# Performance work log

Measured on AMD Instinct MI355X. Metric: run time of the kernel, lower is better.

The kernel has to match this reference:

```python
import jax, jax.numpy as jnp
import numpy as np

N_EMB = 1024
N_HEAD = 16
HEAD_SIZE = N_EMB // N_HEAD  # 64
B, T = 4, 4096


def setup_inputs() -> dict:
    key = jax.random.key(0)
    kx, kq, kk, kv = jax.random.split(key, 4)
    x = jax.random.normal(kx, (B, T, N_EMB), dtype=jnp.float32)
    # torch nn.Linear(in=N_EMB, out=HEAD_SIZE, bias=False) weight: [out, in]
    s = 1.0 / np.sqrt(N_EMB)
    Wq = jax.random.uniform(kq, (HEAD_SIZE, N_EMB), jnp.float32, -s, s)
    Wk = jax.random.uniform(kk, (HEAD_SIZE, N_EMB), jnp.float32, -s, s)
    Wv = jax.random.uniform(kv, (HEAD_SIZE, N_EMB), jnp.float32, -s, s)
    return {"x": x, "Wq": Wq, "Wk": Wk, "Wv": Wv}


def reference(x, Wq, Wk, Wv):
    # q,k,v: [B,T,H]
    q = jnp.einsum('btc,hc->bth', x, Wq)
    k = jnp.einsum('btc,hc->bth', x, Wk)
    v = jnp.einsum('btc,hc->bth', x, Wv)
    scale = HEAD_SIZE ** (-0.5)
    att = jnp.einsum('bth,bsh->bts', q, k) * scale  # [B,T,T]
    Tn = x.shape[1]
    causal = jnp.tril(jnp.ones((Tn, Tn), dtype=bool))
    att = jnp.where(causal, att, -jnp.inf)
    att = jax.nn.softmax(att, axis=-1)
    # dropout p=0.0 -> identity
    out = jnp.einsum('bts,bsh->bth', att, v)  # [B,T,H]
    return out
```

## Files before the change

### kernel.cpp

```cpp
#include <hip/hip_runtime.h>


typedef __attribute__((ext_vector_type(8))) short v8s;
typedef __attribute__((ext_vector_type(4))) float v4f;

static __device__ __forceinline__ unsigned short f2bf(float x) {
  unsigned int u = __builtin_bit_cast(unsigned int, x);
  u += 0x7fffu + ((u >> 16) & 1u);
  return (unsigned short)(u >> 16);
}

static __device__ __forceinline__ void dma16(const void* src, void* dst) {
  __builtin_amdgcn_global_load_lds(
      (const __attribute__((address_space(1))) void*)src,
      (__attribute__((address_space(3))) void*)dst, 16, 0, 0);
}

__global__ __launch_bounds__(256) void pack_w(const float* __restrict__ Wq,
                                              const float* __restrict__ Wk,
                                              const float* __restrict__ Wv,
                                              unsigned short* __restrict__ WF) {
  int idx = (blockIdx.x * 256 + threadIdx.x) * 4;
  int row = idx >> 10;
  int k   = idx & 1023;
  const float* src;
  float scale;
  if (row < 64)       { src = Wq + row * 1024 + k;         scale = 0.125f; }
  else if (row < 128) { src = Wk + (row - 64) * 1024 + k;  scale = 1.0f;   }
  else                { src = Wv + (row - 128) * 1024 + k; scale = 1.0f;   }
  float4 f = *(const float4*)src;
  ushort4 o;
  o.x = f2bf(f.x * scale); o.y = f2bf(f.y * scale);
  o.z = f2bf(f.z * scale); o.w = f2bf(f.w * scale);
  size_t off = ((size_t)(k >> 5) * 12 + (row >> 4)) * 512 +
               (((k >> 3) & 3) * 16 + (row & 15)) * 8 + (k & 7);
  *(ushort4*)(WF + off) = o;
}

__global__ __launch_bounds__(256) void qkv(const float* __restrict__ x,
                                           const unsigned short* __restrict__ WF,
                                           unsigned short* __restrict__ Qg,
                                           unsigned short* __restrict__ KF,
                                           unsigned short* __restrict__ VF) {
  __shared__ alignas(16) char xs[2][32768];
  const int tid   = threadIdx.x;
  const int lane  = tid & 63;
  const int wv    = tid >> 6;
  const int quad  = lane >> 4;
  const int colid = lane & 15;
  const int row0  = blockIdx.x * 64;

  const char* xB = (const char*)x;
  const unsigned short* wf = WF + lane * 8;

  v4f acc[12];
#pragma unroll
  for (int i = 0; i < 12; i++) acc[i] = (v4f){0.f, 0.f, 0.f, 0.f};

  auto stage = [&](int kt, int slot) {
#pragma unroll
    for (int i = 0; i < 8; i++) {
      int id = wv * 8 + i;
      int s = (id >> 1) & 3, h = id & 1;
      const char* src = xB + (size_t)(row0 + wv * 16 + colid) * 4096 +
                        kt * 512 + s * 128 + quad * 32 + h * 16;
      dma16(src, &xs[slot][id * 1024]);
    }
  };

  stage(0, 0);

  for (int kt = 0; kt < 8; kt++) {
    const int slot = kt & 1;
    __syncthreads();
    if (kt < 7) stage(kt + 1, slot ^ 1);
#pragma unroll
    for (int s = 0; s < 4; s++) {
      const int g = kt * 4 + s;
      v8s bw[3];
#pragma unroll
      for (int ntl = 0; ntl < 3; ntl++)
        bw[ntl] = *(const v8s*)(wf + ((size_t)g * 12 + wv * 3 + ntl) * 512);
#pragma unroll
      for (int mg = 0; mg < 4; mg++) {
        float4 f0 = *(const float4*)(&xs[slot][(mg * 8 + s * 2 + 0) * 1024 + lane * 16]);
        float4 f1 = *(const float4*)(&xs[slot][(mg * 8 + s * 2 + 1) * 1024 + lane * 16]);
        v8s a;
        a[0] = (short)f2bf(f0.x); a[1] = (short)f2bf(f0.y);
        a[2] = (short)f2bf(f0.z); a[3] = (short)f2bf(f0.w);
        a[4] = (short)f2bf(f1.x); a[5] = (short)f2bf(f1.y);
        a[6] = (short)f2bf(f1.z); a[7] = (short)f2bf(f1.w);
#pragma unroll
        for (int ntl = 0; ntl < 3; ntl++)
          acc[mg * 3 + ntl] =
              __builtin_amdgcn_mfma_f32_16x16x32_bf16(a, bw[ntl], acc[mg * 3 + ntl], 0, 0, 0);
      }
    }
  }

#pragma unroll
  for (int ntl = 0; ntl < 3; ntl++) {
    const int nt = wv * 3 + ntl;
#pragma unroll
    for (int mg = 0; mg < 4; mg++) {
      const int trow_base = row0 + mg * 16 + quad * 4;
      if (nt < 4) {
#pragma unroll
        for (int r = 0; r < 4; r++)
          Qg[(size_t)(trow_base + r) * 64 + nt * 16 + colid] =
              f2bf(acc[mg * 3 + ntl][r]);
      } else if (nt < 8) {
        int half = (nt - 4) >> 1;
        int q_f  = ((nt - 4) * 2 + (colid >> 3)) & 3;
        int j    = colid & 7;
#pragma unroll
        for (int r = 0; r < 4; r++) {
          int t  = trow_base + r;
          int b  = t >> 12, tl = t & 4095;
          int si = tl >> 6, sl = tl & 63;
          KF[((size_t)(b * 64 + si) * 8 + (sl >> 4) * 2 + half) * 512 +
             (q_f * 16 + (sl & 15)) * 8 + j] = f2bf(acc[mg * 3 + ntl][r]);
        }
      } else {
#pragma unroll
        for (int r = 0; r < 4; r++) {
          int t  = trow_base + r;
          int b  = t >> 12, tl = t & 4095;
          int si = tl >> 6;
          int half = (tl >> 5) & 1, q_f = (tl >> 3) & 3, j = tl & 7;
          VF[((size_t)(b * 64 + si) * 8 + (nt - 8) * 2 + half) * 512 +
             (q_f * 16 + colid) * 8 + j] = f2bf(acc[mg * 3 + ntl][r]);
        }
      }
    }
  }
}

__global__ __launch_bounds__(256, 2) void flash(const unsigned short* __restrict__ Qg,
                                                const unsigned short* __restrict__ KF,
                                                const unsigned short* __restrict__ VF,
                                                float* __restrict__ out) {
  __shared__ alignas(16) char smem[4 * 32 * 68 * 4 + 4 * 32 * 4];
  unsigned short* pl = (unsigned short*)smem;
  float* redf = (float*)smem;
  float* lred = (float*)(smem + 4 * 32 * 68 * 4);

  const int tid   = threadIdx.x;
  const int lane  = tid & 63;
  const int wv    = tid >> 6;
  const int quad  = lane >> 4;
  const int colid = lane & 15;
  const int qt32  = 127 - (int)(blockIdx.x >> 2);
  const int b     = blockIdx.x & 3;
  const int bT    = b * 4096;
  const int row00 = qt32 * 32;
  const int qimax = (row00 + 31) >> 6;

  v8s qf[2][2];
#pragma unroll
  for (int mt = 0; mt < 2; mt++) {
    const unsigned short* qrow =
        Qg + (size_t)(bT + row00 + mt * 16 + colid) * 64 + quad * 8;
    qf[mt][0] = *(const v8s*)(qrow);
    qf[mt][1] = *(const v8s*)(qrow + 32);
  }

  v8s ones;
#pragma unroll
  for (int j = 0; j < 8; j++) ones[j] = (short)0x3F80;

  v4f o[2][4];
#pragma unroll
  for (int mt = 0; mt < 2; mt++)
#pragma unroll
    for (int i = 0; i < 4; i++) o[mt][i] = (v4f){0.f, 0.f, 0.f, 0.f};
  v4f lac[2];
  lac[0] = (v4f){0.f, 0.f, 0.f, 0.f};
  lac[1] = (v4f){0.f, 0.f, 0.f, 0.f};

  const unsigned short* kb0 = KF + (size_t)b * 64 * 4096 + lane * 8;
  const unsigned short* vb0 = VF + (size_t)b * 64 * 4096 + lane * 8;

  for (int si = wv; si <= qimax; si += 4) {
    const unsigned short* ktile = kb0 + (size_t)si * 4096;
    const unsigned short* vtile = vb0 + (size_t)si * 4096;
    v8s ck[8], cv[8];
#pragma unroll
    for (int c = 0; c < 8; c++) ck[c] = *(const v8s*)(ktile + (size_t)c * 512);
#pragma unroll
    for (int c = 0; c < 8; c++) cv[c] = *(const v8s*)(vtile + (size_t)c * 512);

#pragma unroll
    for (int mt = 0; mt < 2; mt++) {
      v4f s[4];
#pragma unroll
      for (int i = 0; i < 4; i++) s[i] = (v4f){0.f, 0.f, 0.f, 0.f};
#pragma unroll
      for (int nt = 0; nt < 4; nt++) {
        s[nt] = __builtin_amdgcn_mfma_f32_16x16x32_bf16(qf[mt][0], ck[2 * nt], s[nt], 0, 0, 0);
        s[nt] = __builtin_amdgcn_mfma_f32_16x16x32_bf16(qf[mt][1], ck[2 * nt + 1], s[nt], 0, 0, 0);
      }

      if (si == qimax) {
        int rowb = row00 + mt * 16 + quad * 4;
        int colb = si * 64;
#pragma unroll
        for (int nt = 0; nt < 4; nt++)
#pragma unroll
          for (int r = 0; r < 4; r++)
            if (colb + nt * 16 + colid > rowb + r) s[nt][r] = -1e30f;
      }

      unsigned short* pw = pl + (wv * 2 + mt) * (16 * 72);
#pragma unroll
      for (int nt = 0; nt < 4; nt++)
#pragma unroll
        for (int r = 0; r < 4; r++)
          pw[(quad * 4 + r) * 72 + nt * 16 + colid] = f2bf(__expf(s[nt][r]));
    }

#pragma unroll
    for (int mt = 0; mt < 2; mt++) {
      unsigned short* pw = pl + (wv * 2 + mt) * (16 * 72);
#pragma unroll
      for (int ks = 0; ks < 64; ks += 32) {
        v8s af = *(const v8s*)(&pw[colid * 72 + ks + quad * 8]);
        lac[mt] = __builtin_amdgcn_mfma_f32_16x16x32_bf16(af, ones, lac[mt], 0, 0, 0);
#pragma unroll
        for (int nt = 0; nt < 4; nt++)
          o[mt][nt] = __builtin_amdgcn_mfma_f32_16x16x32_bf16(
              af, cv[2 * nt + (ks >> 5)], o[mt][nt], 0, 0, 0);
      }
    }
  }

  __syncthreads();
#pragma unroll
  for (int mt = 0; mt < 2; mt++) {
#pragma unroll
    for (int nt = 0; nt < 4; nt++)
#pragma unroll
      for (int r = 0; r < 4; r++)
        redf[(wv * 32 + mt * 16 + quad * 4 + r) * 68 + nt * 16 + colid] = o[mt][nt][r];
    if (colid == 0) {
#pragma unroll
      for (int r = 0; r < 4; r++)
        lred[wv * 32 + mt * 16 + quad * 4 + r] = lac[mt][r];
    }
  }
  __syncthreads();

  {
    int col = tid & 63;
    int r0  = tid >> 6;
#pragma unroll
    for (int rr = 0; rr < 8; rr++) {
      int row = r0 * 8 + rr;
      float sum = 0.f, lsum = 0.f;
#pragma unroll
      for (int w = 0; w < 4; w++) {
        sum  += redf[(w * 32 + row) * 68 + col];
        lsum += lred[w * 32 + row];
      }
      out[(size_t)(bT + row00 + row) * 64 + col] = sum / lsum;
    }
  }
}

extern "C" void kernel_launch(void* const* d_in, const int* in_sizes, int n_in,
                              void* d_out, int out_size, void* d_ws, size_t ws_size,
                              hipStream_t stream) {
  const float* x  = (const float*)d_in[0];
  const float* Wq = (const float*)d_in[1];
  const float* Wk = (const float*)d_in[2];
  const float* Wv = (const float*)d_in[3];
  float* out = (float*)d_out;

  unsigned short* WF = (unsigned short*)d_ws;
  unsigned short* Qg = WF + 192 * 1024;
  unsigned short* KF = Qg + 16384 * 64;
  unsigned short* VF = KF + 16384 * 64;

  hipLaunchKernelGGL(pack_w, dim3(192), dim3(256), 0, stream, Wq, Wk, Wv, WF);
  hipLaunchKernelGGL(qkv, dim3(256), dim3(256), 0, stream, x, WF, Qg, KF, VF);
  hipLaunchKernelGGL(flash, dim3(512), dim3(256), 0, stream, Qg, KF, VF, out);
}
```

Baseline: 136.9 us.

## Split QKV projection into 16-row blocks with full-K XOR-swizzled LDS staging

The QKV projection kernel now handles 16 rows per block instead of 64 and launches 1024 blocks instead of 256, so more CUs are busy. Each block DMA-loads its entire 16x1024 fp32 x slice into 64KB of LDS in one shot, using an XOR swizzle to avoid bank conflicts. The double-buffered K-loop pipeline is removed. The trade-off is that the weight fragments are re-read by four times as many blocks, and there is no overlap between the load and the compute.

```diff
diff --git a/kernel.cpp b/kernel.cpp
--- a/kernel.cpp
+++ b/kernel.cpp
@@ -42,95 +42,82 @@
                                            unsigned short* __restrict__ Qg,
                                            unsigned short* __restrict__ KF,
                                            unsigned short* __restrict__ VF) {
-  __shared__ alignas(16) char xs[2][32768];
+  __shared__ alignas(16) char xs[65536];
   const int tid   = threadIdx.x;
   const int lane  = tid & 63;
   const int wv    = tid >> 6;
   const int quad  = lane >> 4;
   const int colid = lane & 15;
-  const int row0  = blockIdx.x * 64;
-
-  const char* xB = (const char*)x;
+  const int row0  = blockIdx.x * 16;
+
+  const char* xB = (const char*)x + (size_t)blockIdx.x * 65536;
   const unsigned short* wf = WF + lane * 8;
 
-  v4f acc[12];
-#pragma unroll
-  for (int i = 0; i < 12; i++) acc[i] = (v4f){0.f, 0.f, 0.f, 0.f};
-
-  auto stage = [&](int kt, int slot) {
-#pragma unroll
-    for (int i = 0; i < 8; i++) {
-      int id = wv * 8 + i;
-      int s = (id >> 1) & 3, h = id & 1;
-      const char* src = xB + (size_t)(row0 + wv * 16 + colid) * 4096 +
-                        kt * 512 + s * 128 + quad * 32 + h * 16;
-      dma16(src, &xs[slot][id * 1024]);
-    }
-  };
-
-  stage(0, 0);
-
-  for (int kt = 0; kt < 8; kt++) {
-    const int slot = kt & 1;
-    __syncthreads();
-    if (kt < 7) stage(kt + 1, slot ^ 1);
-#pragma unroll
-    for (int s = 0; s < 4; s++) {
-      const int g = kt * 4 + s;
-      v8s bw[3];
-#pragma unroll
-      for (int ntl = 0; ntl < 3; ntl++)
-        bw[ntl] = *(const v8s*)(wf + ((size_t)g * 12 + wv * 3 + ntl) * 512);
-#pragma unroll
-      for (int mg = 0; mg < 4; mg++) {
-        float4 f0 = *(const float4*)(&xs[slot][(mg * 8 + s * 2 + 0) * 1024 + lane * 16]);
-        float4 f1 = *(const float4*)(&xs[slot][(mg * 8 + s * 2 + 1) * 1024 + lane * 16]);
-        v8s a;
-        a[0] = (short)f2bf(f0.x); a[1] = (short)f2bf(f0.y);
-        a[2] = (short)f2bf(f0.z); a[3] = (short)f2bf(f0.w);
-        a[4] = (short)f2bf(f1.x); a[5] = (short)f2bf(f1.y);
-        a[6] = (short)f2bf(f1.z); a[7] = (short)f2bf(f1.w);
-#pragma unroll
-        for (int ntl = 0; ntl < 3; ntl++)
-          acc[mg * 3 + ntl] =
-              __builtin_amdgcn_mfma_f32_16x16x32_bf16(a, bw[ntl], acc[mg * 3 + ntl], 0, 0, 0);
-      }
-    }
-  }
-
+  const int l8 = lane & ~7, l7 = lane & 7;
+#pragma unroll
+  for (int i = 0; i < 16; i++) {
+    int j   = wv * 16 + i;
+    int key = (j >> 2) & 7;
+    const char* src = xB + (size_t)j * 1024 + (l8 | (l7 ^ key)) * 16;
+    dma16(src, &xs[j * 1024]);
+  }
+  __syncthreads();
+
+  v4f acc[3];
+#pragma unroll
+  for (int i = 0; i < 3; i++) acc[i] = (v4f){0.f, 0.f, 0.f, 0.f};
+
+  const int c7 = colid & 7;
+#pragma unroll 4
+  for (int g = 0; g < 32; g++) {
+    v8s bw[3];
+#pragma unroll
+    for (int ntl = 0; ntl < 3; ntl++)
+      bw[ntl] = *(const v8s*)(wf + ((size_t)g * 12 + wv * 3 + ntl) * 512);
+    int ug  = g * 8 + quad * 2;
+    int su0 = (ug & ~7) | ((ug & 7) ^ c7);
+    int su1 = (ug & ~7) | (((ug & 7) + 1) ^ c7);
+    float4 f0 = *(const float4*)(&xs[colid * 4096 + su0 * 16]);
+    float4 f1 = *(const float4*)(&xs[colid * 4096 + su1 * 16]);
+    v8s a;
+    a[0] = (short)f2bf(f0.x); a[1] = (short)f2bf(f0.y);
+    a[2] = (short)f2bf(f0.z); a[3] = (short)f2bf(f0.w);
+    a[4] = (short)f2bf(f1.x); a[5] = (short)f2bf(f1.y);
+    a[6] = (short)f2bf(f1.z); a[7] = (short)f2bf(f1.w);
+#pragma unroll
+    for (int ntl = 0; ntl < 3; ntl++)
+      acc[ntl] = __builtin_amdgcn_mfma_f32_16x16x32_bf16(a, bw[ntl], acc[ntl], 0, 0, 0);
+  }
+
+  const int trow_base = row0 + quad * 4;
 #pragma unroll
   for (int ntl = 0; ntl < 3; ntl++) {
     const int nt = wv * 3 + ntl;
-#pragma unroll
-    for (int mg = 0; mg < 4; mg++) {
-      const int trow_base = row0 + mg * 16 + quad * 4;
-      if (nt < 4) {
-#pragma unroll
-        for (int r = 0; r < 4; r++)
-          Qg[(size_t)(trow_base + r) * 64 + nt * 16 + colid] =
-              f2bf(acc[mg * 3 + ntl][r]);
-      } else if (nt < 8) {
-        int half = (nt - 4) >> 1;
-        int q_f  = ((nt - 4) * 2 + (colid >> 3)) & 3;
-        int j    = colid & 7;
-#pragma unroll
-        for (int r = 0; r < 4; r++) {
-          int t  = trow_base + r;
-          int b  = t >> 12, tl = t & 4095;
-          int si = tl >> 6, sl = tl & 63;
-          KF[((size_t)(b * 64 + si) * 8 + (sl >> 4) * 2 + half) * 512 +
-             (q_f * 16 + (sl & 15)) * 8 + j] = f2bf(acc[mg * 3 + ntl][r]);
-        }
-      } else {
-#pragma unroll
-        for (int r = 0; r < 4; r++) {
-          int t  = trow_base + r;
-          int b  = t >> 12, tl = t & 4095;
-          int si = tl >> 6;
-          int half = (tl >> 5) & 1, q_f = (tl >> 3) & 3, j = tl & 7;
-          VF[((size_t)(b * 64 + si) * 8 + (nt - 8) * 2 + half) * 512 +
-             (q_f * 16 + colid) * 8 + j] = f2bf(acc[mg * 3 + ntl][r]);
-        }
+    if (nt < 4) {
+#pragma unroll
+      for (int r = 0; r < 4; r++)
+        Qg[(size_t)(trow_base + r) * 64 + nt * 16 + colid] = f2bf(acc[ntl][r]);
+    } else if (nt < 8) {
+      int half = (nt - 4) >> 1;
+      int q_f  = ((nt - 4) * 2 + (colid >> 3)) & 3;
+      int j    = colid & 7;
+#pragma unroll
+      for (int r = 0; r < 4; r++) {
+        int t  = trow_base + r;
+        int b  = t >> 12, tl = t & 4095;
+        int si = tl >> 6, sl = tl & 63;
+        KF[((size_t)(b * 64 + si) * 8 + (sl >> 4) * 2 + half) * 512 +
+           (q_f * 16 + (sl & 15)) * 8 + j] = f2bf(acc[ntl][r]);
+      }
+    } else {
+#pragma unroll
+      for (int r = 0; r < 4; r++) {
+        int t  = trow_base + r;
+        int b  = t >> 12, tl = t & 4095;
+        int si = tl >> 6;
+        int half = (tl >> 5) & 1, q_f = (tl >> 3) & 3, j = tl & 7;
+        VF[((size_t)(b * 64 + si) * 8 + (nt - 8) * 2 + half) * 512 +
+           (q_f * 16 + colid) * 8 + j] = f2bf(acc[ntl][r]);
       }
     }
   }
@@ -282,6 +269,6 @@
   unsigned short* VF = KF + 16384 * 64;
 
   hipLaunchKernelGGL(pack_w, dim3(192), dim3(256), 0, stream, Wq, Wk, Wv, WF);
-  hipLaunchKernelGGL(qkv, dim3(256), dim3(256), 0, stream, x, WF, Qg, KF, VF);
+  hipLaunchKernelGGL(qkv, dim3(1024), dim3(256), 0, stream, x, WF, Qg, KF, VF);
   hipLaunchKernelGGL(flash, dim3(512), dim3(256), 0, stream, Qg, KF, VF, out);
 }
```

Result: faster. 132.5 us (-3.2%).
